# Kernel tuning notes

Hardware: AMD Instinct MI355X
Metric: run time of the kernel (lower is better)

## Reference

```python
import jax, jax.numpy as jnp
import numpy as np

N = 100000
E = 1600000
IN, HID, OUT = 512, 256, 32
K = 3
LAMBDA_AMP = 0.5


def setup_inputs() -> dict:
    key = jax.random.key(0)
    ks = jax.random.split(key, 6)
    x = jax.random.normal(ks[0], (N, IN), dtype=jnp.float32)
    edge_index = jax.random.randint(ks[1], (2, E), 0, N, dtype=jnp.int64)
    # MLP params (PyTorch Linear default init: U(-1/sqrt(fan_in), 1/sqrt(fan_in)))
    s1 = 1.0 / np.sqrt(IN)
    W1 = jax.random.uniform(ks[2], (IN, HID), jnp.float32, -s1, s1)
    b1 = jax.random.uniform(ks[3], (HID,), jnp.float32, -s1, s1)
    s2 = 1.0 / np.sqrt(HID)
    W2 = jax.random.uniform(ks[4], (HID, OUT), jnp.float32, -s2, s2)
    b2 = jax.random.uniform(ks[5], (OUT,), jnp.float32, -s2, s2)
    return {"x": x, "W1": W1, "b1": b1, "W2": W2, "b2": b2, "edge_index": edge_index}


def _gcn_norm(edge_index, n_nodes, dtype):
    # add self loops, symmetric normalization D^-1/2 (A+I) D^-1/2
    loop = jnp.arange(n_nodes, dtype=edge_index.dtype)
    row = jnp.concatenate([edge_index[0], loop])
    col = jnp.concatenate([edge_index[1], loop])
    w = jnp.ones(row.shape[0], dtype=dtype)
    deg = jax.ops.segment_sum(w, col, num_segments=n_nodes)
    dis = jnp.where(deg > 0, jax.lax.rsqrt(deg), 0.0)
    norm = dis[row] * w * dis[col]
    return row, col, norm


def _proximal_l21(x, lam):
    # row-wise soft-thresholding of L2 norms
    rn = jnp.sqrt(jnp.sum(x * x, axis=1))  # [N]
    safe = jnp.where(rn > 0, rn, 1.0)
    score = jnp.where(rn > 0, jnp.maximum(rn - lam, 0.0) / safe, 0.0)
    return score[:, None] * x


def reference(x, W1, b1, W2, b2, edge_index):
    # MLP (dropout inactive at inference)
    h = jax.nn.relu(x @ W1 + b1)
    h = h @ W2 + b2  # [N, OUT]

    row, col, norm = _gcn_norm(edge_index, N, h.dtype)

    lam = LAMBDA_AMP
    gamma = 1.0 / (2.0 * (1.0 - lam))
    hh = h
    xk = h
    for _ in range(K):
        # A_hat @ xk via gather-scale-scatter
        ax = jax.ops.segment_sum(norm[:, None] * xk[row], col, num_segments=N)
        lx = xk - ax  # L @ xk
        y = xk - gamma * 2.0 * (1.0 - lam) * lx
        xk = hh + _proximal_l21(y - hh, lam * gamma)
    return xk
```

## Files before the change

kernel.cpp:

```cpp
#include <hip/hip_runtime.h>
#include <cstdint>

#define NN 100000
#define EE 1600000
#define IN_F 512
#define HID_F 256
#define OUT_F 32
#define GSL 256
#define SLICE_W 12500
#define CAP 64

typedef float f32x4 __attribute__((ext_vector_type(4)));
typedef int   i32x4 __attribute__((ext_vector_type(4)));
typedef short s16x8 __attribute__((ext_vector_type(8)));
typedef unsigned short u16;

static __device__ __forceinline__ u16 f2bf(float f) {
  uint32_t u = __builtin_bit_cast(uint32_t, f);
  u += 0x7FFFu + ((u >> 16) & 1u);
  return (u16)(u >> 16);
}

static __device__ __forceinline__ float bf2f(u16 v) {
  uint32_t u = ((uint32_t)v) << 16;
  return __builtin_bit_cast(float, u);
}

static __device__ __forceinline__ uint32_t pk_bf16(float a, float b) {
  uint32_t r;
  asm("v_cvt_pk_bf16_f32 %0, %1, %2" : "=v"(r) : "v"(a), "v"(b));
  return r;
}

__global__ __launch_bounds__(256) void k_prep(const float* __restrict__ w1,
                                              u16* __restrict__ w1s,
                                              const float* __restrict__ w2,
                                              u16* __restrict__ w2s,
                                              int* __restrict__ cur) {
  int b = blockIdx.x;
  int tid = threadIdx.x;
  if (b < 512) {
    int g = b * 256 + tid;
    int kt = g >> 14;
    int r  = g & 16383;
    int n  = r >> 6;
    int jp = r & 63;
    int kb = (jp * 2) ^ ((n & 7) << 4);
    int k  = kt * 64 + (kb >> 1);
    w1s[g] = f2bf(w1[k * HID_F + n]);
  } else if (b < 544) {
    int g = (b - 512) * 256 + tid;
    int n  = g >> 8;
    int jp = g & 255;
    int kb = (jp * 2) ^ ((n & 7) << 4);
    int j  = kb >> 1;
    w2s[g] = f2bf(w2[j * OUT_F + n]);
  } else {
    int i = (b - 544) * 256 + tid;
    if (i < NN) cur[i] = 0;
  }
}

__global__ __launch_bounds__(256) void k_fillC(const int* __restrict__ row,
                                               const int* __restrict__ col,
                                               int* __restrict__ cur,
                                               int* __restrict__ csr) {
  const int slice = blockIdx.x & 7;
  const int g = blockIdx.x >> 3;
  const unsigned lo = (unsigned)slice * SLICE_W, hi = lo + SLICE_W;
  const i32x4* c4 = (const i32x4*)col;
  const i32x4* r4 = (const i32x4*)row;
  for (int i = g * 256 + threadIdx.x; i < EE / 4; i += GSL * 256) {
    i32x4 c = c4[i];
    i32x4 r = r4[i];
    #pragma unroll
    for (int k = 0; k < 4; ++k) {
      unsigned cc = (unsigned)c[k];
      if (cc >= lo && cc < hi) {
        int p = atomicAdd(&cur[cc], 1);
        if (p < CAP) csr[(int)cc * CAP + p] = r[k];
      }
    }
  }
}

__global__ __launch_bounds__(512) void k_mlp(
    const float* __restrict__ x, const float* __restrict__ b1,
    const float* __restrict__ b2, const u16* __restrict__ w1s,
    const u16* __restrict__ w2s, const int* __restrict__ cnt,
    float* __restrict__ hout, u16* __restrict__ xs0) {
  __shared__ char smem[81920];
  char* aL  = smem;
  char* bL  = smem + 16384;
  char* h1L = smem;
  char* w2L = smem + 65536;

  const int tid  = threadIdx.x;
  const int lane = tid & 63;
  const int wid  = tid >> 6;
  const int wm   = wid >> 2;
  const int wn   = wid & 3;
  const int l16  = lane & 15;
  const int lq   = lane >> 4;
  const int row0 = blockIdx.x * 128;

  {
    const char* src = (const char*)w2s;
    #pragma unroll
    for (int p = 0; p < 2; ++p) {
      int off = (p * 512 + tid) * 16;
      *(f32x4*)(w2L + off) = *(const f32x4*)(src + off);
    }
  }

  const f32x4 zf = {0.f, 0.f, 0.f, 0.f};
  f32x4 acc[4][4];
  #pragma unroll
  for (int i = 0; i < 4; ++i)
    #pragma unroll
    for (int j = 0; j < 4; ++j) acc[i][j] = zf;

  for (int kt = 0; kt < IN_F / 64; ++kt) {
    __syncthreads();
    #pragma unroll
    for (int p = 0; p < 4; ++p) {
      int v   = p * 512 + tid;
      int row = v >> 4;
      int f4  = v & 15;
      int grow = row0 + row;
      f32x4 xv = zf;
      if (grow < NN)
        xv = *(const f32x4*)(x + (size_t)grow * IN_F + kt * 64 + f4 * 4);
      uint32_t lo = pk_bf16(xv.x, xv.y);
      uint32_t hi = pk_bf16(xv.z, xv.w);
      uint64_t wv = (uint64_t)lo | ((uint64_t)hi << 32);
      int kb = (f4 * 8) ^ ((row & 7) << 4);
      *(uint64_t*)(aL + row * 128 + kb) = wv;
    }
    {
      const char* src = (const char*)w1s + kt * 32768;
      #pragma unroll
      for (int p = 0; p < 4; ++p) {
        int off = (p * 512 + tid) * 16;
        *(f32x4*)(bL + off) = *(const f32x4*)(src + off);
      }
    }
    __syncthreads();
    #pragma unroll
    for (int ks = 0; ks < 2; ++ks) {
      int kb = ks * 64 + lq * 16;
      s16x8 af[4], bf[4];
      #pragma unroll
      for (int fm = 0; fm < 4; ++fm) {
        int row = wm * 64 + fm * 16 + l16;
        af[fm] = *(const s16x8*)(aL + row * 128 + (kb ^ ((row & 7) << 4)));
      }
      #pragma unroll
      for (int fn = 0; fn < 4; ++fn) {
        int n = wn * 64 + fn * 16 + l16;
        bf[fn] = *(const s16x8*)(bL + n * 128 + (kb ^ ((n & 7) << 4)));
      }
      #pragma unroll
      for (int fm = 0; fm < 4; ++fm)
        #pragma unroll
        for (int fn = 0; fn < 4; ++fn)
          acc[fm][fn] = __builtin_amdgcn_mfma_f32_16x16x32_bf16(
              af[fm], bf[fn], acc[fm][fn], 0, 0, 0);
    }
  }

  float b1v[4];
  #pragma unroll
  for (int fn = 0; fn < 4; ++fn) b1v[fn] = b1[wn * 64 + fn * 16 + l16];

  __syncthreads();
  #pragma unroll
  for (int fm = 0; fm < 4; ++fm) {
    #pragma unroll
    for (int fn = 0; fn < 4; ++fn) {
      int col = wn * 64 + fn * 16 + l16;
      #pragma unroll
      for (int r = 0; r < 4; ++r) {
        int row = wm * 64 + fm * 16 + lq * 4 + r;
        float v = acc[fm][fn][r] + b1v[fn];
        v = fmaxf(v, 0.f);
        *(u16*)(h1L + row * 512 + ((col * 2) ^ ((row & 7) << 4))) = f2bf(v);
      }
    }
  }
  __syncthreads();

  f32x4 acc2[2];
  acc2[0] = zf; acc2[1] = zf;
  const int arow = wid * 16 + l16;
  #pragma unroll
  for (int ks = 0; ks < 8; ++ks) {
    int kb = ks * 64 + lq * 16;
    s16x8 af = *(const s16x8*)(h1L + arow * 512 + (kb ^ ((arow & 7) << 4)));
    #pragma unroll
    for (int fn = 0; fn < 2; ++fn) {
      int bn = fn * 16 + l16;
      s16x8 bf = *(const s16x8*)(w2L + bn * 512 + (kb ^ ((bn & 7) << 4)));
      acc2[fn] = __builtin_amdgcn_mfma_f32_16x16x32_bf16(af, bf, acc2[fn], 0, 0, 0);
    }
  }
  #pragma unroll
  for (int r = 0; r < 4; ++r) {
    int row = row0 + wid * 16 + lq * 4 + r;
    if (row >= NN) continue;
    float dr = rsqrtf((float)cnt[row] + 1.0f);
    #pragma unroll
    for (int fn = 0; fn < 2; ++fn) {
      int col = fn * 16 + l16;
      float v = acc2[fn][r] + b2[col];
      hout[(size_t)row * 32 + col] = v;
      xs0[(size_t)row * 32 + col] = f2bf(dr * v);
    }
  }
}

template <int LAST>
__global__ __launch_bounds__(256) void k_prop(
    const u16* __restrict__ xs, const float* __restrict__ hh,
    u16* __restrict__ xs_out, float* __restrict__ fout,
    const int* __restrict__ cnt, const int* __restrict__ csr) {
  int w = blockIdx.x * 4 + (threadIdx.x >> 6);
  if (w >= NN) return;
  const int lane = threadIdx.x & 63;
  const int q = lane & 3;
  const int s = lane >> 2;
  const int n = cnt[w];
  const int* __restrict__ crow = csr + (size_t)w * CAP;
  float acc[8] = {0.f, 0.f, 0.f, 0.f, 0.f, 0.f, 0.f, 0.f};
  for (int j = s; j < n; j += 16) {
    int src = crow[j];
    s16x8 v = *(const s16x8*)(xs + (size_t)src * 32 + q * 8);
    #pragma unroll
    for (int k = 0; k < 8; ++k) acc[k] += bf2f((u16)v[k]);
  }
  if (s == 0) {
    s16x8 v = *(const s16x8*)(xs + (size_t)w * 32 + q * 8);
    #pragma unroll
    for (int k = 0; k < 8; ++k) acc[k] += bf2f((u16)v[k]);
  }
  #pragma unroll
  for (int m = 4; m <= 32; m <<= 1) {
    #pragma unroll
    for (int k = 0; k < 8; ++k) acc[k] += __shfl_xor(acc[k], m, 64);
  }
  const float di = rsqrtf((float)n + 1.0f);
  const f32x4 h0 = *(const f32x4*)(hh + (size_t)w * 32 + q * 8);
  const f32x4 h1 = *(const f32x4*)(hh + (size_t)w * 32 + q * 8 + 4);
  float hv[8] = {h0.x, h0.y, h0.z, h0.w, h1.x, h1.y, h1.z, h1.w};
  float d[8];
  float rn2 = 0.f;
  #pragma unroll
  for (int k = 0; k < 8; ++k) {
    d[k] = di * acc[k] - hv[k];
    rn2 += d[k] * d[k];
  }
  rn2 += __shfl_xor(rn2, 1, 64);
  rn2 += __shfl_xor(rn2, 2, 64);
  float rn = sqrtf(rn2);
  float sc = (rn > 0.f) ? fmaxf(rn - 0.5f, 0.f) / rn : 0.f;
  if (s == 0) {
    if (LAST) {
      f32x4 o0, o1;
      o0.x = hv[0] + sc * d[0]; o0.y = hv[1] + sc * d[1];
      o0.z = hv[2] + sc * d[2]; o0.w = hv[3] + sc * d[3];
      o1.x = hv[4] + sc * d[4]; o1.y = hv[5] + sc * d[5];
      o1.z = hv[6] + sc * d[6]; o1.w = hv[7] + sc * d[7];
      *(f32x4*)(fout + (size_t)w * 32 + q * 8) = o0;
      *(f32x4*)(fout + (size_t)w * 32 + q * 8 + 4) = o1;
    } else {
      s16x8 o;
      #pragma unroll
      for (int k = 0; k < 8; ++k) o[k] = (short)f2bf(di * (hv[k] + sc * d[k]));
      *(s16x8*)(xs_out + (size_t)w * 32 + q * 8) = o;
    }
  }
}

extern "C" void kernel_launch(void* const* d_in, const int* in_sizes, int n_in,
                              void* d_out, int out_size, void* d_ws, size_t ws_size,
                              hipStream_t stream) {
  const float* x  = (const float*)d_in[0];
  const float* W1 = (const float*)d_in[1];
  const float* b1 = (const float*)d_in[2];
  const float* W2 = (const float*)d_in[3];
  const float* b2 = (const float*)d_in[4];
  const int*   ei = (const int*)d_in[5];

  char* ws = (char*)d_ws;
  float* h    = (float*)(ws);
  u16*   xs0  = (u16*)  (ws + 12800000);
  u16*   xs1  = (u16*)  (ws + 19200000);
  int*   csr  = (int*)  (ws + 25600000);
  int*   cur  = (int*)  (ws + 51200000);
  u16*   w1s  = (u16*)  (ws + 51600000);
  u16*   w2s  = (u16*)  (ws + 51862144);

  k_prep<<<935, 256, 0, stream>>>(W1, w1s, W2, w2s, cur);
  k_fillC<<<8 * GSL, 256, 0, stream>>>(ei, ei + EE, cur, csr);
  k_mlp<<<(NN + 127) / 128, 512, 0, stream>>>(x, b1, b2, w1s, w2s, cur, h, xs0);

  float* out = (float*)d_out;
  k_prop<0><<<(NN + 3) / 4, 256, 0, stream>>>(xs0, h, xs1, nullptr, cur, csr);
  k_prop<0><<<(NN + 3) / 4, 256, 0, stream>>>(xs1, h, xs0, nullptr, cur, csr);
  k_prop<1><<<(NN + 3) / 4, 256, 0, stream>>>(xs0, h, nullptr, out,  cur, csr);
}
```

Measured before the change: 276.5 us.

## Load MLP operands directly from global into MFMA fragments, dropping LDS staging

```diff
diff --git a/kernel.cpp b/kernel.cpp
--- a/kernel.cpp
+++ b/kernel.cpp
@@ -13,6 +13,7 @@
 typedef float f32x4 __attribute__((ext_vector_type(4)));
 typedef int   i32x4 __attribute__((ext_vector_type(4)));
 typedef short s16x8 __attribute__((ext_vector_type(8)));
+typedef uint32_t u32x4 __attribute__((ext_vector_type(4)));
 typedef unsigned short u16;
 
 static __device__ __forceinline__ u16 f2bf(float f) {
@@ -41,12 +42,13 @@
   int tid = threadIdx.x;
   if (b < 512) {
     int g = b * 256 + tid;
-    int kt = g >> 14;
-    int r  = g & 16383;
-    int n  = r >> 6;
-    int jp = r & 63;
-    int kb = (jp * 2) ^ ((n & 7) << 4);
-    int k  = kt * 64 + (kb >> 1);
+    int j    = g & 7;
+    int lane = (g >> 3) & 63;
+    int fnG  = (g >> 9) & 15;
+    int kk   = g >> 13;
+    int l16 = lane & 15, lq = lane >> 4;
+    int k = (kk >> 1) * 64 + (kk & 1) * 32 + lq * 8 + j;
+    int n = fnG * 16 + l16;
     w1s[g] = f2bf(w1[k * HID_F + n]);
   } else if (b < 544) {
     int g = (b - 512) * 256 + tid;
@@ -90,8 +92,6 @@
     const u16* __restrict__ w2s, const int* __restrict__ cnt,
     float* __restrict__ hout, u16* __restrict__ xs0) {
   __shared__ char smem[81920];
-  char* aL  = smem;
-  char* bL  = smem + 16384;
   char* h1L = smem;
   char* w2L = smem + 65536;
 
@@ -120,45 +120,33 @@
     #pragma unroll
     for (int j = 0; j < 4; ++j) acc[i][j] = zf;
 
+  const int arow_base = row0 + wm * 64;
+
   for (int kt = 0; kt < IN_F / 64; ++kt) {
-    __syncthreads();
-    #pragma unroll
-    for (int p = 0; p < 4; ++p) {
-      int v   = p * 512 + tid;
-      int row = v >> 4;
-      int f4  = v & 15;
-      int grow = row0 + row;
-      f32x4 xv = zf;
-      if (grow < NN)
-        xv = *(const f32x4*)(x + (size_t)grow * IN_F + kt * 64 + f4 * 4);
-      uint32_t lo = pk_bf16(xv.x, xv.y);
-      uint32_t hi = pk_bf16(xv.z, xv.w);
-      uint64_t wv = (uint64_t)lo | ((uint64_t)hi << 32);
-      int kb = (f4 * 8) ^ ((row & 7) << 4);
-      *(uint64_t*)(aL + row * 128 + kb) = wv;
-    }
-    {
-      const char* src = (const char*)w1s + kt * 32768;
-      #pragma unroll
-      for (int p = 0; p < 4; ++p) {
-        int off = (p * 512 + tid) * 16;
-        *(f32x4*)(bL + off) = *(const f32x4*)(src + off);
-      }
-    }
-    __syncthreads();
     #pragma unroll
     for (int ks = 0; ks < 2; ++ks) {
-      int kb = ks * 64 + lq * 16;
+      const int kcol = kt * 64 + ks * 32 + lq * 8;
       s16x8 af[4], bf[4];
       #pragma unroll
+      for (int fn = 0; fn < 4; ++fn) {
+        const u16* src = w1s + ((size_t)(((kt * 2 + ks) * 16) + wn * 4 + fn) * 64 + lane) * 8;
+        bf[fn] = *(const s16x8*)src;
+      }
+      #pragma unroll
       for (int fm = 0; fm < 4; ++fm) {
-        int row = wm * 64 + fm * 16 + l16;
-        af[fm] = *(const s16x8*)(aL + row * 128 + (kb ^ ((row & 7) << 4)));
-      }
-      #pragma unroll
-      for (int fn = 0; fn < 4; ++fn) {
-        int n = wn * 64 + fn * 16 + l16;
-        bf[fn] = *(const s16x8*)(bL + n * 128 + (kb ^ ((n & 7) << 4)));
+        int grow = arow_base + fm * 16 + l16;
+        f32x4 a0 = zf, a1 = zf;
+        if (grow < NN) {
+          const float* xp = x + (size_t)grow * IN_F + kcol;
+          a0 = *(const f32x4*)xp;
+          a1 = *(const f32x4*)(xp + 4);
+        }
+        u32x4 pk;
+        pk.x = pk_bf16(a0.x, a0.y);
+        pk.y = pk_bf16(a0.z, a0.w);
+        pk.z = pk_bf16(a1.x, a1.y);
+        pk.w = pk_bf16(a1.z, a1.w);
+        af[fm] = __builtin_bit_cast(s16x8, pk);
       }
       #pragma unroll
       for (int fm = 0; fm < 4; ++fm)
@@ -173,7 +161,6 @@
   #pragma unroll
   for (int fn = 0; fn < 4; ++fn) b1v[fn] = b1[wn * 64 + fn * 16 + l16];
 
-  __syncthreads();
   #pragma unroll
   for (int fm = 0; fm < 4; ++fm) {
     #pragma unroll
```

New measurement: 364.2 us. +31.7%, slower.
